# Performance work log

Hardware: AMD Instinct MI355X
Metric: run time of the kernel (lower is better)

Reference implementation:

```python
import jax, jax.numpy as jnp
import numpy as np

NUM_HEADS = 8
ALPHA = 0.01  # leaky_relu slope
MAX_SEQ = 64


def layer_norm(x, g, b, eps=1e-5):
    m = jnp.mean(x, axis=-1, keepdims=True)
    v = jnp.var(x, axis=-1, keepdims=True)
    return (x - m) * jax.lax.rsqrt(v + eps) * g + b


def ff(x, w1, b1, w2, b2):
    # Linear -> exact GELU -> Linear (torch nn.GELU default is erf-based)
    return jax.nn.gelu(x @ w1.T + b1, approximate=False) @ w2.T + b2


def mha(q, k, v, in_w, in_b, out_w, out_b, kpm):
    # torch nn.MultiheadAttention, batch_first=False. q:[Tq,E,d], k/v:[Tk,E,d], kpm:[E,Tk] True=pad
    d = q.shape[-1]
    H = NUM_HEADS
    dh = d // H
    qp = q @ in_w[:d].T + in_b[:d]
    kp = k @ in_w[d:2 * d].T + in_b[d:2 * d]
    vp = v @ in_w[2 * d:].T + in_b[2 * d:]
    Tq, E, _ = qp.shape
    Tk = kp.shape[0]
    qh = qp.reshape(Tq, E, H, dh) * (dh ** -0.5)
    kh = kp.reshape(Tk, E, H, dh)
    vh = vp.reshape(Tk, E, H, dh)
    scores = jnp.einsum('qehd,kehd->ehqk', qh, kh)  # [E,H,Tq,Tk]
    scores = jnp.where(kpm[:, None, None, :], jnp.float32(-1e9), scores)
    att = jax.nn.softmax(scores, axis=-1)
    out = jnp.einsum('ehqk,kehd->qehd', att, vh).reshape(Tq, E, d)
    return out @ out_w.T + out_b


def setup_inputs() -> dict:
    key = jax.random.key(0)
    ks = jax.random.split(key, 40)
    N, d, E, Seq, H = 50000, 64, 150000, 5, NUM_HEADS

    def xn(k, shape, scale):
        return jax.random.normal(k, shape, dtype=jnp.float32) * scale

    inp = {
        'features': xn(ks[0], (N, d), 1.0),
        'pos_emb': xn(ks[1], (MAX_SEQ, d), 0.02),
        'self_in_w': xn(ks[2], (3 * d, d), 0.1),
        'self_in_b': jnp.zeros((3 * d,), jnp.float32),
        'self_out_w': xn(ks[3], (d, d), 0.1),
        'self_out_b': jnp.zeros((d,), jnp.float32),
        'cross_in_w': xn(ks[4], (3 * d, d), 0.1),
        'cross_in_b': jnp.zeros((3 * d,), jnp.float32),
        'cross_out_w': xn(ks[5], (d, d), 0.1),
        'cross_out_b': jnp.zeros((d,), jnp.float32),
        'sa_ln1_g': jnp.ones((d,), jnp.float32), 'sa_ln1_b': jnp.zeros((d,), jnp.float32),
        'sa_ln2_g': jnp.ones((d,), jnp.float32), 'sa_ln2_b': jnp.zeros((d,), jnp.float32),
        'ca_ln1_g': jnp.ones((d,), jnp.float32), 'ca_ln1_b': jnp.zeros((d,), jnp.float32),
        'ca_ln2_g': jnp.ones((d,), jnp.float32), 'ca_ln2_b': jnp.zeros((d,), jnp.float32),
        'sa_ff_w1': xn(ks[6], (4 * d, d), 0.08), 'sa_ff_b1': jnp.zeros((4 * d,), jnp.float32),
        'sa_ff_w2': xn(ks[7], (d, 4 * d), 0.08), 'sa_ff_b2': jnp.zeros((d,), jnp.float32),
        'ca_ff_w1': xn(ks[8], (4 * d, d), 0.08), 'ca_ff_b1': jnp.zeros((4 * d,), jnp.float32),
        'ca_ff_w2': xn(ks[9], (d, 4 * d), 0.08), 'ca_ff_b2': jnp.zeros((d,), jnp.float32),
        'inst_w': xn(ks[10], (NUM_HEADS * d, d), 0.08),
        'attn_vec': xn(ks[11], (1, NUM_HEADS, d), 0.2),
        'edge_metapath_indices': jax.random.randint(ks[12], (E, Seq), 0, N, dtype=jnp.int64)
            if jax.config.jax_enable_x64 else jax.random.randint(ks[12], (E, Seq), 0, N).astype(jnp.int32),
        'dst': jax.random.randint(ks[13], (E,), 0, N).astype(jnp.int32),
    }
    inp['edge_metapath_indices'] = inp['edge_metapath_indices'].astype(jnp.int32)
    return inp


def reference(features, pos_emb, self_in_w, self_in_b, self_out_w, self_out_b,
              cross_in_w, cross_in_b, cross_out_w, cross_out_b,
              sa_ln1_g, sa_ln1_b, sa_ln2_g, sa_ln2_b,
              ca_ln1_g, ca_ln1_b, ca_ln2_g, ca_ln2_b,
              sa_ff_w1, sa_ff_b1, sa_ff_w2, sa_ff_b2,
              ca_ff_w1, ca_ff_b1, ca_ff_w2, ca_ff_b2,
              inst_w, attn_vec, edge_metapath_indices, dst):
    N, d = features.shape
    pad_id = N  # module pads one zero row; indices == pad_id are padding
    feats = jnp.concatenate([features, jnp.zeros((1, d), features.dtype)], axis=0)
    idx = edge_metapath_indices  # [E, Seq]
    E, Seq = idx.shape
    kpm = idx == pad_id  # [E, Seq] key padding mask

    edata = feats[idx]  # [E, Seq, d] gather (embedding)
    tokens = jnp.transpose(edata, (1, 0, 2))  # [Seq, E, d]
    pos_vec = pos_emb[:Seq][:, None, :]  # [Seq, 1, d]
    pos_vec = jnp.where(kpm.T[:, :, None], jnp.float32(0.0), pos_vec)
    tokens = tokens + pos_vec  # pos_drop is identity in eval

    # pre-LN self-attention block over the metapath sequence
    sa_in = layer_norm(tokens, sa_ln1_g, sa_ln1_b)
    tokens = tokens + mha(sa_in, sa_in, sa_in, self_in_w, self_in_b, self_out_w, self_out_b, kpm)
    sa_out = jnp.transpose(tokens, (1, 0, 2))  # [E, Seq, d]

    valid = (~kpm).astype(features.dtype)  # [E, Seq]
    denom = jnp.clip(valid.sum(axis=1, keepdims=True), 1.0, None)
    inst_emb = (sa_out * valid[:, :, None]).sum(axis=1) / denom  # masked mean pool
    inst_emb = inst_emb + ff(layer_norm(inst_emb, sa_ln2_g, sa_ln2_b), sa_ff_w1, sa_ff_b1, sa_ff_w2, sa_ff_b2)

    # cross-attention: last (target) node attends over the sequence
    lengths = (~kpm).sum(axis=1)
    last_pos = jnp.clip(lengths - 1, 0, None)
    last_ids = jnp.take_along_axis(idx, last_pos[:, None], axis=1)[:, 0]
    target_feat = feats[last_ids]
    q = layer_norm(target_feat, ca_ln1_g, ca_ln1_b)[None]  # [1, E, d]
    cross_out = mha(q, tokens, tokens, cross_in_w, cross_in_b, cross_out_w, cross_out_b, kpm)
    inst_emb = inst_emb + cross_out[0]
    inst_emb = inst_emb + ff(layer_norm(inst_emb, ca_ln2_g, ca_ln2_b), ca_ff_w1, ca_ff_b1, ca_ff_w2, ca_ff_b2)

    # heads projection, leaky-relu attention score, edge softmax, scatter-sum
    eft = (inst_emb @ inst_w.T).reshape(E, NUM_HEADS, d)  # [E, H, d]
    a = jnp.sum(eft * attn_vec, axis=-1)  # [E, H]
    a = jnp.where(a > 0, a, ALPHA * a)  # leaky_relu
    seg_max = jax.ops.segment_max(a, dst, num_segments=N)  # per-dst-node max
    a_exp = jnp.exp(a - seg_max[dst])
    seg_sum = jax.ops.segment_sum(a_exp, dst, num_segments=N)
    att = a_exp / seg_sum[dst]  # edge_softmax; attn_drop=0 -> identity
    ret = jax.ops.segment_sum(eft * att[:, :, None], dst, num_segments=N)  # [N, H, d]
    return ret
```

## Files before the change

### kernel.cpp

```cpp
#include <hip/hip_runtime.h>
#include <math.h>

#define D 64
#define LOG2E 1.44269504088896340736f
#define QSCALE (0.35355339059327373f * LOG2E)

typedef float f32x4 __attribute__((ext_vector_type(4)));
typedef float vf4 __attribute__((ext_vector_type(4)));
typedef short bf16x8 __attribute__((ext_vector_type(8)));
typedef unsigned short ushort_t;
typedef unsigned int uint2v __attribute__((ext_vector_type(2)));

#define MF(a, b, c) __builtin_amdgcn_mfma_f32_16x16x32_bf16(a, b, c, 0, 0, 0)

__device__ __forceinline__ float bcast(float x, int i) {
  return __int_as_float(__builtin_amdgcn_readlane(__float_as_int(x), i));
}

__device__ __forceinline__ float xs16(float x) {
#if __has_builtin(__builtin_amdgcn_permlane16_swap)
  uint2v a = __builtin_amdgcn_permlane16_swap(__float_as_uint(x), __float_as_uint(x), false, false);
  return __uint_as_float(a[0]) + __uint_as_float(a[1]);
#else
  return x + __shfl_xor(x, 16);
#endif
}
__device__ __forceinline__ float xs32(float x) {
#if __has_builtin(__builtin_amdgcn_permlane32_swap)
  uint2v a = __builtin_amdgcn_permlane32_swap(__float_as_uint(x), __float_as_uint(x), false, false);
  return __uint_as_float(a[0]) + __uint_as_float(a[1]);
#else
  return x + __shfl_xor(x, 32);
#endif
}
__device__ __forceinline__ float qsum(float x) {
  return xs32(xs16(x));
}

__device__ __forceinline__ ushort_t f2b(float f) {
  unsigned int u = __float_as_uint(f);
  unsigned int r = (u + 0x7FFFu + ((u >> 16) & 1u)) >> 16;
  return (ushort_t)r;
}
__device__ __forceinline__ unsigned int pkrtne(float lo, float hi) {
  unsigned int a = __float_as_uint(lo);
  unsigned int b = __float_as_uint(hi);
  a = a + 0x7FFFu + ((a >> 16) & 1u);
  b = b + 0x7FFFu + ((b >> 16) & 1u);
  return __builtin_amdgcn_perm(b, a, 0x07060302u);
}
__device__ __forceinline__ f32x4 ld4(const float* __restrict__ p) { return *(const f32x4*)p; }
__device__ __forceinline__ bf16x8 mkpair(const f32x4& ce, const f32x4& co) {
  union { bf16x8 v; unsigned int w[4]; } u;
  u.w[0] = pkrtne(ce[0], ce[1]);
  u.w[1] = pkrtne(ce[2], ce[3]);
  u.w[2] = pkrtne(co[0], co[1]);
  u.w[3] = pkrtne(co[2], co[3]);
  return u.v;
}
__device__ __forceinline__ f32x4 unpk(bf16x8 p, int half) {
  union { bf16x8 v; unsigned int w[4]; } u;
  u.v = p;
  unsigned int w0 = u.w[half * 2], w1 = u.w[half * 2 + 1];
  f32x4 r;
  r[0] = __uint_as_float(w0 << 16);
  r[1] = __uint_as_float(w0 & 0xFFFF0000u);
  r[2] = __uint_as_float(w1 << 16);
  r[3] = __uint_as_float(w1 & 0xFFFF0000u);
  return r;
}

__device__ __forceinline__ void lnT(const f32x4 (&x)[4], f32x4 (&y)[4],
                                    const float* __restrict__ g, const float* __restrict__ b,
                                    int quad) {
  float s1 = 0.f, s2 = 0.f;
#pragma unroll
  for (int ct = 0; ct < 4; ct++)
#pragma unroll
    for (int r = 0; r < 4; r++) { s1 += x[ct][r]; s2 += x[ct][r] * x[ct][r]; }
  s1 = qsum(s1);
  s2 = qsum(s2);
  float mean = s1 * 0.015625f;
  float var = s2 * 0.015625f - mean * mean;
  float rs = rsqrtf(var + 1e-5f);
#pragma unroll
  for (int ct = 0; ct < 4; ct++) {
    f32x4 gv = ld4(g + 16 * ct + 4 * quad);
    f32x4 bv = ld4(b + 16 * ct + 4 * quad);
#pragma unroll
    for (int r = 0; r < 4; r++) y[ct][r] = (x[ct][r] - mean) * rs * gv[r] + bv[r];
  }
}

__global__ void prep_kernel(const float* __restrict__ si, const float* __restrict__ so,
                            const float* __restrict__ w1s, const float* __restrict__ w2s,
                            const float* __restrict__ ci, const float* __restrict__ co,
                            const float* __restrict__ w1c, const float* __restrict__ w2c,
                            const float* __restrict__ iw, const float* __restrict__ av,
                            float* __restrict__ ws, unsigned int* __restrict__ zp, int zn) {
  int t = blockIdx.x * blockDim.x + threadIdx.x;
  ushort_t* bw = (ushort_t*)(ws + 33280);
  if (t < 98304) {
    const float* src;
    int base, cs;
    int l = t;
    if      (l < 12288) { src = si;  base = 0;     cs = 6; }
    else if (l < 16384) { src = so;  base = 12288; cs = 6; l -= 12288; }
    else if (l < 32768) { src = w1s; base = 16384; cs = 6; l -= 16384; }
    else if (l < 49152) { src = w2s; base = 32768; cs = 8; l -= 32768; }
    else if (l < 61440) { src = ci;  base = 49152; cs = 6; l -= 49152; }
    else if (l < 65536) { src = co;  base = 61440; cs = 6; l -= 61440; }
    else if (l < 81920) { src = w1c; base = 65536; cs = 6; l -= 65536; }
    else                { src = w2c; base = 81920; cs = 8; l -= 81920; }
    int c = l >> cs, k = l & ((1 << cs) - 1);
    int T = (1 << cs) >> 5;
    int ct = c >> 4, m = c & 15, tt = k >> 5, rem = k & 31;
    int quad = (rem >> 2) & 3;
    int j = (((rem >> 4) & 1) << 2) | (rem & 3);
    bw[base + (size_t)((ct * T + tt) * 64 + quad * 16 + m) * 8 + j] = f2b(src[l]);
  } else if (t < 131072) {
    int l = t - 98304;
    int c = l >> 6, k = l & 63;
    ws[(k >> 2) * 2048 + c * 4 + (k & 3)] = iw[l];
  } else if (t < 131584) {
    int l = t - 131072;
    int h = l >> 6, k = l & 63;
    float acc = 0.f;
    for (int c = 0; c < 64; c++) acc += av[h * 64 + c] * iw[(h * 64 + c) * 64 + k];
    ws[32768 + h * 64 + k] = acc;
  } else if (t - 131584 < zn) {
    zp[t - 131584] = 0u;
  }
}

#define SC1(KARR, QF, CT, KS, P)                                                        \
  { f32x4 kv_ = unpk(KARR[KS][(CT) >> 1], (CT) & 1);                                    \
    float sp_ = QF[CT][0] * kv_[0] + QF[CT][1] * kv_[1] + QF[CT][2] * kv_[2] +          \
                QF[CT][3] * kv_[3];                                                     \
    sp_ = xs16(sp_);                                                                    \
    P = ((vb >> (KS)) & 1) ? sp_ : -1e30f; }

#define PV1(VARR, CT, KS, P, ACC)                                                       \
  { f32x4 vv_ = unpk(VARR[KS][(CT) >> 1], (CT) & 1);                                    \
    _Pragma("unroll") for (int r = 0; r < 4; r++) ACC[r] = fmaf(P, vv_[r], ACC[r]); }

#define ATT_CT(KARR, VARR, QF, CT, OD)                                                  \
  {                                                                                     \
    float p0, p1, p2, p3, p4;                                                           \
    SC1(KARR, QF, CT, 0, p0); SC1(KARR, QF, CT, 1, p1); SC1(KARR, QF, CT, 2, p2);       \
    SC1(KARR, QF, CT, 3, p3); SC1(KARR, QF, CT, 4, p4);                                 \
    float mx_ = fmaxf(fmaxf(fmaxf(p0, p1), fmaxf(p2, p3)), p4);                         \
    p0 = exp2f(p0 - mx_); p1 = exp2f(p1 - mx_); p2 = exp2f(p2 - mx_);                   \
    p3 = exp2f(p3 - mx_); p4 = exp2f(p4 - mx_);                                         \
    float ri_ = 1.0f / (p0 + p1 + p2 + p3 + p4);                                        \
    p0 *= ri_; p1 *= ri_; p2 *= ri_; p3 *= ri_; p4 *= ri_;                              \
    OD = (f32x4){0.f, 0.f, 0.f, 0.f};                                                   \
    PV1(VARR, CT, 0, p0, OD); PV1(VARR, CT, 1, p1, OD); PV1(VARR, CT, 2, p2, OD);       \
    PV1(VARR, CT, 3, p3, OD); PV1(VARR, CT, 4, p4, OD);                                 \
  }

#define KV_STAGE(S)                                                                     \
  {                                                                                     \
    f32x4 t[4], y[4];                                                                   \
    const bool vd = (vb >> (S)) & 1;                                                    \
    const float* fp = features + (size_t)min(ids[S], N - 1) * 64;                       \
    _Pragma("unroll")                                                                   \
    for (int ct = 0; ct < 4; ct++) {                                                    \
      f32x4 f = ld4(fp + 16 * ct + 4 * quad);                                           \
      f32x4 pv = ld4(pos_emb + (S) * 64 + 16 * ct + 4 * quad);                          \
      _Pragma("unroll")                                                                 \
      for (int r = 0; r < 4; r++) t[ct][r] = vd ? (f[r] + pv[r]) : 0.f;                 \
    }                                                                                   \
    lnT(t, y, sa_ln1_g, sa_ln1_b, quad);                                                \
    bf16x8 xl0 = mkpair(y[0], y[1]), xl1 = mkpair(y[2], y[3]);                          \
    f32x4 kt[4], vt[4];                                                                 \
    _Pragma("unroll")                                                                   \
    for (int ct = 0; ct < 4; ct++) {                                                    \
      f32x4 c = {0.f, 0.f, 0.f, 0.f};                                                   \
      c = MF(WSI[((4 + ct) * 2 + 0) * 64 + lane], xl0, c);                              \
      c = MF(WSI[((4 + ct) * 2 + 1) * 64 + lane], xl1, c);                              \
      f32x4 bb = ld4(self_in_b + 64 + 16 * ct + 4 * quad);                              \
      _Pragma("unroll")                                                                 \
      for (int r = 0; r < 4; r++) kt[ct][r] = c[r] + bb[r];                             \
      f32x4 c2 = {0.f, 0.f, 0.f, 0.f};                                                  \
      c2 = MF(WSI[((8 + ct) * 2 + 0) * 64 + lane], xl0, c2);                            \
      c2 = MF(WSI[((8 + ct) * 2 + 1) * 64 + lane], xl1, c2);                            \
      f32x4 bb2 = ld4(self_in_b + 128 + 16 * ct + 4 * quad);                            \
      _Pragma("unroll")                                                                 \
      for (int r = 0; r < 4; r++) vt[ct][r] = c2[r] + bb2[r];                           \
    }                                                                                   \
    Kp[S][0] = mkpair(kt[0], kt[1]); Kp[S][1] = mkpair(kt[2], kt[3]);                   \
    Vp[S][0] = mkpair(vt[0], vt[1]); Vp[S][1] = mkpair(vt[2], vt[3]);                   \
  }

#define Q_STAGE(S)                                                                      \
  {                                                                                     \
    const bool vd = (vb >> (S)) & 1;                                                    \
    const float* fp = features + (size_t)min(ids[S], N - 1) * 64;                       \
    f32x4 t[4], y[4];                                                                   \
    _Pragma("unroll")                                                                   \
    for (int ct = 0; ct < 4; ct++) {                                                    \
      f32x4 f = ld4(fp + 16 * ct + 4 * quad);                                           \
      f32x4 pv = ld4(pos_emb + (S) * 64 + 16 * ct + 4 * quad);                          \
      _Pragma("unroll")                                                                 \
      for (int r = 0; r < 4; r++) t[ct][r] = vd ? (f[r] + pv[r]) : 0.f;                 \
    }                                                                                   \
    lnT(t, y, sa_ln1_g, sa_ln1_b, quad);                                                \
    bf16x8 xl0 = mkpair(y[0], y[1]), xl1 = mkpair(y[2], y[3]);                          \
    f32x4 qf[4];                                                                        \
    _Pragma("unroll")                                                                   \
    for (int ct = 0; ct < 4; ct++) {                                                    \
      f32x4 c = {0.f, 0.f, 0.f, 0.f};                                                   \
      c = MF(WSI[(ct * 2 + 0) * 64 + lane], xl0, c);                                    \
      c = MF(WSI[(ct * 2 + 1) * 64 + lane], xl1, c);                                    \
      f32x4 bb = ld4(self_in_b + 16 * ct + 4 * quad);                                   \
      _Pragma("unroll")                                                                 \
      for (int r = 0; r < 4; r++) qf[ct][r] = (c[r] + bb[r]) * QSCALE;                  \
    }                                                                                   \
    f32x4 oa0, oa1, oa2, oa3;                                                           \
    ATT_CT(Kp, Vp, qf, 0, oa0); ATT_CT(Kp, Vp, qf, 1, oa1);                             \
    ATT_CT(Kp, Vp, qf, 2, oa2); ATT_CT(Kp, Vp, qf, 3, oa3);                             \
    bf16x8 op0 = mkpair(oa0, oa1), op1 = mkpair(oa2, oa3);                              \
    f32x4 tpc[4];                                                                       \
    _Pragma("unroll")                                                                   \
    for (int ct = 0; ct < 4; ct++) {                                                    \
      f32x4 c = {0.f, 0.f, 0.f, 0.f};                                                   \
      c = MF(WSO[(ct * 2 + 0) * 64 + lane], op0, c);                                    \
      c = MF(WSO[(ct * 2 + 1) * 64 + lane], op1, c);                                    \
      f32x4 bb = ld4(self_out_b + 16 * ct + 4 * quad);                                  \
      _Pragma("unroll")                                                                 \
      for (int r = 0; r < 4; r++) {                                                     \
        float tp_ = c[r] + bb[r] + t[ct][r];                                            \
        tpc[ct][r] = tp_;                                                               \
        pool[ct][r] += vd ? tp_ : 0.f;                                                  \
      }                                                                                 \
    }                                                                                   \
    TP[S][0] = mkpair(tpc[0], tpc[1]); TP[S][1] = mkpair(tpc[2], tpc[3]);               \
  }

#define CKV_STAGE(S)                                                                    \
  {                                                                                     \
    f32x4 kt[4], vt[4];                                                                 \
    _Pragma("unroll")                                                                   \
    for (int ct = 0; ct < 4; ct++) {                                                    \
      f32x4 c = {0.f, 0.f, 0.f, 0.f};                                                   \
      c = MF(WCI[((4 + ct) * 2 + 0) * 64 + lane], TP[S][0], c);                         \
      c = MF(WCI[((4 + ct) * 2 + 1) * 64 + lane], TP[S][1], c);                         \
      f32x4 bb = ld4(cross_in_b + 64 + 16 * ct + 4 * quad);                             \
      _Pragma("unroll")                                                                 \
      for (int r = 0; r < 4; r++) kt[ct][r] = c[r] + bb[r];                             \
      f32x4 c2 = {0.f, 0.f, 0.f, 0.f};                                                  \
      c2 = MF(WCI[((8 + ct) * 2 + 0) * 64 + lane], TP[S][0], c2);                       \
      c2 = MF(WCI[((8 + ct) * 2 + 1) * 64 + lane], TP[S][1], c2);                       \
      f32x4 bb2 = ld4(cross_in_b + 128 + 16 * ct + 4 * quad);                           \
      _Pragma("unroll")                                                                 \
      for (int r = 0; r < 4; r++) vt[ct][r] = c2[r] + bb2[r];                           \
    }                                                                                   \
    Kc[S][0] = mkpair(kt[0], kt[1]); Kc[S][1] = mkpair(kt[2], kt[3]);                   \
    Vc[S][0] = mkpair(vt[0], vt[1]); Vc[S][1] = mkpair(vt[2], vt[3]);                   \
  }

#define FF_H2(CT, HD)                                                                   \
  { f32x4 c = {0.f, 0.f, 0.f, 0.f};                                                     \
    c = MF(W1[((CT) * 2 + 0) * 64 + lane], x0, c);                                      \
    c = MF(W1[((CT) * 2 + 1) * 64 + lane], x1, c);                                      \
    f32x4 bb = ld4(b1 + 16 * (CT) + 4 * quad);                                          \
    _Pragma("unroll")                                                                   \
    for (int r = 0; r < 4; r++) {                                                       \
      float v = c[r] + bb[r];                                                           \
      HD[r] = 0.5f * v * (1.0f + erff(v * 0.70710678118654752440f));                    \
    } }

#define FF_O(CT)                                                                        \
  { f32x4 c = {0.f, 0.f, 0.f, 0.f};                                                     \
    c = MF(W2[((CT) * 8 + 0) * 64 + lane], Hp0, c);                                     \
    c = MF(W2[((CT) * 8 + 1) * 64 + lane], Hp1, c);                                     \
    c = MF(W2[((CT) * 8 + 2) * 64 + lane], Hp2, c);                                     \
    c = MF(W2[((CT) * 8 + 3) * 64 + lane], Hp3, c);                                     \
    c = MF(W2[((CT) * 8 + 4) * 64 + lane], Hp4, c);                                     \
    c = MF(W2[((CT) * 8 + 5) * 64 + lane], Hp5, c);                                     \
    c = MF(W2[((CT) * 8 + 6) * 64 + lane], Hp6, c);                                     \
    c = MF(W2[((CT) * 8 + 7) * 64 + lane], Hp7, c);                                     \
    f32x4 bb = ld4(b2 + 16 * (CT) + 4 * quad);                                          \
    _Pragma("unroll")                                                                   \
    for (int r = 0; r < 4; r++) inst[CT][r] += c[r] + bb[r]; }

__device__ __forceinline__ void ffnT(f32x4 (&inst)[4],
                                     const float* __restrict__ g, const float* __restrict__ b,
                                     const bf16x8* __restrict__ W1, const bf16x8* __restrict__ W2,
                                     const float* __restrict__ b1, const float* __restrict__ b2,
                                     int lane, int quad) {
  f32x4 y[4];
  lnT(inst, y, g, b, quad);
  bf16x8 x0 = mkpair(y[0], y[1]), x1 = mkpair(y[2], y[3]);
  f32x4 ha, hb;
  FF_H2(0, ha);  FF_H2(1, hb);  bf16x8 Hp0 = mkpair(ha, hb);
  FF_H2(2, ha);  FF_H2(3, hb);  bf16x8 Hp1 = mkpair(ha, hb);
  FF_H2(4, ha);  FF_H2(5, hb);  bf16x8 Hp2 = mkpair(ha, hb);
  FF_H2(6, ha);  FF_H2(7, hb);  bf16x8 Hp3 = mkpair(ha, hb);
  FF_H2(8, ha);  FF_H2(9, hb);  bf16x8 Hp4 = mkpair(ha, hb);
  FF_H2(10, ha); FF_H2(11, hb); bf16x8 Hp5 = mkpair(ha, hb);
  FF_H2(12, ha); FF_H2(13, hb); bf16x8 Hp6 = mkpair(ha, hb);
  FF_H2(14, ha); FF_H2(15, hb); bf16x8 Hp7 = mkpair(ha, hb);
  FF_O(0); FF_O(1); FF_O(2); FF_O(3);
}

#define ASC(H)                                                                          \
  { float sp = 0.f;                                                                     \
    _Pragma("unroll")                                                                   \
    for (int ct = 0; ct < 4; ct++) {                                                    \
      f32x4 uu = ld4(uvec + (H) * 64 + 16 * ct + 4 * quad);                             \
      _Pragma("unroll")                                                                 \
      for (int r = 0; r < 4; r++) sp = fmaf(inst[ct][r], uu[r], sp);                    \
    }                                                                                   \
    sp = qsum(sp);                                                                      \
    a##H = sp > 0.f ? sp : 0.01f * sp; }

__global__ __launch_bounds__(64, 1)
void edge_kernel(const float* __restrict__ features, const float* __restrict__ pos_emb,
                 const float* __restrict__ self_in_b, const float* __restrict__ self_out_b,
                 const float* __restrict__ cross_in_b, const float* __restrict__ cross_out_b,
                 const float* __restrict__ sa_ln1_g, const float* __restrict__ sa_ln1_b,
                 const float* __restrict__ sa_ln2_g, const float* __restrict__ sa_ln2_b,
                 const float* __restrict__ ca_ln1_g, const float* __restrict__ ca_ln1_b,
                 const float* __restrict__ ca_ln2_g, const float* __restrict__ ca_ln2_b,
                 const float* __restrict__ sa_ff_b1, const float* __restrict__ sa_ff_b2,
                 const float* __restrict__ ca_ff_b1, const float* __restrict__ ca_ff_b2,
                 const int* __restrict__ midx, const int* __restrict__ dstv,
                 const float* __restrict__ ws,
                 float* __restrict__ inst_out, float* __restrict__ a_out, int E, int N) {
  const int lane = threadIdx.x;
  const int quad = lane >> 4, lo = lane & 15;
  const int e0 = blockIdx.x * 16;
  __shared__ float xp[16 * 68];

  const ushort_t* bw = (const ushort_t*)(ws + 33280);
  const bf16x8* WSI = (const bf16x8*)(bw);
  const bf16x8* WSO = (const bf16x8*)(bw + 12288);
  const bf16x8* W1S = (const bf16x8*)(bw + 16384);
  const bf16x8* W2S = (const bf16x8*)(bw + 32768);
  const bf16x8* WCI = (const bf16x8*)(bw + 49152);
  const bf16x8* WCO = (const bf16x8*)(bw + 61440);
  const bf16x8* W1C = (const bf16x8*)(bw + 65536);
  const bf16x8* W2C = (const bf16x8*)(bw + 81920);
  const float* uvec = ws + 32768;

  const bool ge = (e0 + lo) < E;
  const int eIdx = min(e0 + lo, E - 1);
  int ids[5];
  ids[0] = midx[eIdx * 5 + 0];
  ids[1] = midx[eIdx * 5 + 1];
  ids[2] = midx[eIdx * 5 + 2];
  ids[3] = midx[eIdx * 5 + 3];
  ids[4] = midx[eIdx * 5 + 4];
  int vb = 0;
  if (ids[0] != N && ge) vb |= 1;
  if (ids[1] != N && ge) vb |= 2;
  if (ids[2] != N && ge) vb |= 4;
  if (ids[3] != N && ge) vb |= 8;
  if (ids[4] != N && ge) vb |= 16;
  const int nv = __popc(vb);
  const int lp = max(nv - 1, 0);
  int lid = ids[0];
  lid = (lp == 1) ? ids[1] : lid;
  lid = (lp == 2) ? ids[2] : lid;
  lid = (lp == 3) ? ids[3] : lid;
  lid = (lp == 4) ? ids[4] : lid;

  bf16x8 Kp[5][2], Vp[5][2];
  KV_STAGE(0); KV_STAGE(1); KV_STAGE(2); KV_STAGE(3); KV_STAGE(4);

  f32x4 pool[4];
#pragma unroll
  for (int ct = 0; ct < 4; ct++) pool[ct] = (f32x4){0.f, 0.f, 0.f, 0.f};
  bf16x8 TP[5][2];
  Q_STAGE(0); Q_STAGE(1); Q_STAGE(2); Q_STAGE(3); Q_STAGE(4);

  f32x4 inst[4];
  {
    float rn = 1.0f / (float)max(nv, 1);
#pragma unroll
    for (int ct = 0; ct < 4; ct++)
#pragma unroll
      for (int r = 0; r < 4; r++) inst[ct][r] = pool[ct][r] * rn;
  }

  ffnT(inst, sa_ln2_g, sa_ln2_b, W1S, W2S, sa_ff_b1, sa_ff_b2, lane, quad);

  {
    f32x4 tf[4], xq[4];
    const bool vdl = lid != N;
    const float* fp = features + (size_t)min(lid, N - 1) * 64;
#pragma unroll
    for (int ct = 0; ct < 4; ct++) {
      f32x4 f = ld4(fp + 16 * ct + 4 * quad);
#pragma unroll
      for (int r = 0; r < 4; r++) tf[ct][r] = vdl ? f[r] : 0.f;
    }
    lnT(tf, xq, ca_ln1_g, ca_ln1_b, quad);
    bf16x8 xq0 = mkpair(xq[0], xq[1]), xq1 = mkpair(xq[2], xq[3]);
    f32x4 qcf[4];
#pragma unroll
    for (int ct = 0; ct < 4; ct++) {
      f32x4 c = {0.f, 0.f, 0.f, 0.f};
      c = MF(WCI[(ct * 2 + 0) * 64 + lane], xq0, c);
      c = MF(WCI[(ct * 2 + 1) * 64 + lane], xq1, c);
      f32x4 bb = ld4(cross_in_b + 16 * ct + 4 * quad);
#pragma unroll
      for (int r = 0; r < 4; r++) qcf[ct][r] = (c[r] + bb[r]) * QSCALE;
    }
    bf16x8 Kc[5][2], Vc[5][2];
    CKV_STAGE(0); CKV_STAGE(1); CKV_STAGE(2); CKV_STAGE(3); CKV_STAGE(4);
    f32x4 cc0, cc1, cc2, cc3;
    ATT_CT(Kc, Vc, qcf, 0, cc0); ATT_CT(Kc, Vc, qcf, 1, cc1);
    ATT_CT(Kc, Vc, qcf, 2, cc2); ATT_CT(Kc, Vc, qcf, 3, cc3);
    bf16x8 cp0 = mkpair(cc0, cc1), cp1 = mkpair(cc2, cc3);
#pragma unroll
    for (int ct = 0; ct < 4; ct++) {
      f32x4 c = {0.f, 0.f, 0.f, 0.f};
      c = MF(WCO[(ct * 2 + 0) * 64 + lane], cp0, c);
      c = MF(WCO[(ct * 2 + 1) * 64 + lane], cp1, c);
      f32x4 bb = ld4(cross_out_b + 16 * ct + 4 * quad);
#pragma unroll
      for (int r = 0; r < 4; r++) inst[ct][r] += c[r] + bb[r];
    }
  }

  ffnT(inst, ca_ln2_g, ca_ln2_b, W1C, W2C, ca_ff_b1, ca_ff_b2, lane, quad);

  float a0, a1, a2, a3, a4, a5, a6, a7;
  ASC(0); ASC(1); ASC(2); ASC(3); ASC(4); ASC(5); ASC(6); ASC(7);
  if (ge && quad < 2) {
    f32x4 st = (quad == 0) ? (f32x4){a0, a1, a2, a3} : (f32x4){a4, a5, a6, a7};
    *(f32x4*)(a_out + (size_t)(e0 + lo) * 8 + 4 * quad) = st;
  }

#pragma unroll
  for (int ct = 0; ct < 4; ct++)
    *(f32x4*)(&xp[lo * 68 + 16 * ct + 4 * quad]) = inst[ct];
  __syncthreads();
  {
    int er = lane >> 2, cb = (lane & 3) * 16;
    if (e0 + er < E) {
#pragma unroll
      for (int u = 0; u < 4; u++) {
        f32x4 v = *(const f32x4*)(&xp[er * 68 + cb + 4 * u]);
        *(f32x4*)(inst_out + (size_t)(e0 + er) * 64 + cb + 4 * u) = v;
      }
    }
  }
}

__global__ void csr_count_kernel(const int* __restrict__ dstv, unsigned int* __restrict__ cnt,
                                 int E) {
  int e = blockIdx.x * blockDim.x + threadIdx.x;
  if (e < E) atomicAdd(&cnt[dstv[e]], 1u);
}

__global__ void scan1_kernel(unsigned int* __restrict__ off, unsigned int* __restrict__ bsum,
                             int N) {
  __shared__ unsigned int sd[256];
  int t = threadIdx.x, n = blockIdx.x * 256 + t;
  unsigned int v = (n < N) ? off[n] : 0u;
  sd[t] = v;
  __syncthreads();
  for (int o = 1; o < 256; o <<= 1) {
    unsigned int x = (t >= o) ? sd[t - o] : 0u;
    __syncthreads();
    sd[t] += x;
    __syncthreads();
  }
  if (n < N) off[n] = sd[t] - v;
  if (t == 255) bsum[blockIdx.x] = sd[255];
}

__global__ void scan2_kernel(unsigned int* __restrict__ bsum, int nb) {
  __shared__ unsigned int sd[1024];
  int t = threadIdx.x;
  unsigned int v = (t < nb) ? bsum[t] : 0u;
  sd[t] = v;
  __syncthreads();
  for (int o = 1; o < 1024; o <<= 1) {
    unsigned int x = (t >= o) ? sd[t - o] : 0u;
    __syncthreads();
    sd[t] += x;
    __syncthreads();
  }
  if (t < nb) bsum[t] = sd[t] - v;
}

__global__ void scan3_kernel(unsigned int* __restrict__ off, unsigned int* __restrict__ cur,
                             const unsigned int* __restrict__ bsum, int N, int E) {
  int n = blockIdx.x * 256 + threadIdx.x;
  if (n < N) {
    unsigned int o = off[n] + bsum[blockIdx.x];
    off[n] = o;
    cur[n] = o;
  }
  if (n == 0) off[N] = (unsigned int)E;
}

__global__ void csr_fill_kernel(const int* __restrict__ dstv, unsigned int* __restrict__ cur,
                                unsigned int* __restrict__ elist, int E) {
  int e = blockIdx.x * blockDim.x + threadIdx.x;
  if (e < E) {
    unsigned int p = atomicAdd(&cur[dstv[e]], 1u);
    elist[p] = (unsigned int)e;
  }
}

__global__ __launch_bounds__(256)
void att_kernel(const unsigned int* __restrict__ off, const unsigned int* __restrict__ elist,
                float* __restrict__ a, float* __restrict__ sinv, int N) {
  int n = blockIdx.x * blockDim.x + threadIdx.x;
  if (n >= N) return;
  const unsigned int s0 = off[n], s1 = off[n + 1];
  f32x4 m0 = {-3.0e38f, -3.0e38f, -3.0e38f, -3.0e38f}, m1 = m0;
  for (unsigned int i = s0; i < s1; i++) {
    const float* ap = a + (size_t)elist[i] * 8;
    f32x4 x0 = ld4(ap), x1 = ld4(ap + 4);
#pragma unroll
    for (int r = 0; r < 4; r++) { m0[r] = fmaxf(m0[r], x0[r]); m1[r] = fmaxf(m1[r], x1[r]); }
  }
  f32x4 t0 = {0.f, 0.f, 0.f, 0.f}, t1 = t0;
  for (unsigned int i = s0; i < s1; i++) {
    float* ap = a + (size_t)elist[i] * 8;
    f32x4 x0 = ld4(ap), x1 = ld4(ap + 4);
    f32x4 w0, w1;
#pragma unroll
    for (int r = 0; r < 4; r++) {
      w0[r] = __expf(x0[r] - m0[r]);
      w1[r] = __expf(x1[r] - m1[r]);
      t0[r] += w0[r];
      t1[r] += w1[r];
    }
    *(f32x4*)ap = w0;
    *(f32x4*)(ap + 4) = w1;
  }
  f32x4 r0, r1;
#pragma unroll
  for (int r = 0; r < 4; r++) {
    r0[r] = (t0[r] > 0.f) ? 1.0f / t0[r] : 0.f;
    r1[r] = (t1[r] > 0.f) ? 1.0f / t1[r] : 0.f;
  }
  *(f32x4*)(sinv + (size_t)n * 8) = r0;
  *(f32x4*)(sinv + (size_t)n * 8 + 4) = r1;
}

__global__ __launch_bounds__(256)
void gather_kernel(const float* __restrict__ T_iw, const unsigned int* __restrict__ off,
                   const unsigned int* __restrict__ elist, const float* __restrict__ a,
                   const float* __restrict__ sinv, const float* __restrict__ inst_emb,
                   float* __restrict__ out, int N) {
  const int lane = threadIdx.x & 63;
  const int widx = threadIdx.x >> 6;
  const int h = blockIdx.y;
  const vf4* P = (const vf4*)T_iw;
  vf4 wr[16];
#pragma unroll
  for (int k = 0; k < 16; k++) wr[k] = P[k * 512 + h * 64 + lane];
  const int stride = gridDim.x * 4;
  for (int n = blockIdx.x * 4 + widx; n < N; n += stride) {
    const unsigned int s0 = off[n], s1 = off[n + 1];
    float z = 0.f;
    for (unsigned int i = s0; i < s1; i++) {
      unsigned int e = elist[i];
      z = fmaf(a[(size_t)e * 8 + h], inst_emb[(size_t)e * 64 + lane], z);
    }
    z *= sinv[(size_t)n * 8 + h];
    float o = 0.f;
#pragma unroll
    for (int k = 0; k < 16; k++) {
#pragma unroll
      for (int u = 0; u < 4; u++) o = fmaf(bcast(z, k * 4 + u), wr[k][u], o);
    }
    out[(size_t)n * 512 + h * 64 + lane] = o;
  }
}

extern "C" void kernel_launch(void* const* d_in, const int* in_sizes, int n_in,
                              void* d_out, int out_size, void* d_ws, size_t ws_size,
                              hipStream_t stream) {
  const float* features   = (const float*)d_in[0];
  const float* pos_emb    = (const float*)d_in[1];
  const float* self_in_w  = (const float*)d_in[2];
  const float* self_in_b  = (const float*)d_in[3];
  const float* self_out_w = (const float*)d_in[4];
  const float* self_out_b = (const float*)d_in[5];
  const float* cross_in_w = (const float*)d_in[6];
  const float* cross_in_b = (const float*)d_in[7];
  const float* cross_out_w= (const float*)d_in[8];
  const float* cross_out_b= (const float*)d_in[9];
  const float* sa_ln1_g = (const float*)d_in[10];
  const float* sa_ln1_b = (const float*)d_in[11];
  const float* sa_ln2_g = (const float*)d_in[12];
  const float* sa_ln2_b = (const float*)d_in[13];
  const float* ca_ln1_g = (const float*)d_in[14];
  const float* ca_ln1_b = (const float*)d_in[15];
  const float* ca_ln2_g = (const float*)d_in[16];
  const float* ca_ln2_b = (const float*)d_in[17];
  const float* sa_ff_w1 = (const float*)d_in[18];
  const float* sa_ff_b1 = (const float*)d_in[19];
  const float* sa_ff_w2 = (const float*)d_in[20];
  const float* sa_ff_b2 = (const float*)d_in[21];
  const float* ca_ff_w1 = (const float*)d_in[22];
  const float* ca_ff_b1 = (const float*)d_in[23];
  const float* ca_ff_w2 = (const float*)d_in[24];
  const float* ca_ff_b2 = (const float*)d_in[25];
  const float* inst_w   = (const float*)d_in[26];
  const float* attn_vec = (const float*)d_in[27];
  const int* midx = (const int*)d_in[28];
  const int* dstv = (const int*)d_in[29];

  const int N = in_sizes[0] / 64;
  const int E = in_sizes[29];

  float* wsf = (float*)d_ws;
  float* inst_emb = wsf + 131072;
  float* a_arr = inst_emb + (size_t)E * 64;
  unsigned int* off = (unsigned int*)(a_arr + (size_t)E * 8);
  unsigned int* cur = off + (size_t)(N + 1);
  unsigned int* bsum = cur + (size_t)N;
  unsigned int* elist = bsum + 1024;
  float* sinv = (float*)(elist + (size_t)E);

  const int nb1 = (N + 255) / 256;

  int zn = N + 1;
  prep_kernel<<<(131584 + zn + 255) / 256, 256, 0, stream>>>(
      self_in_w, self_out_w, sa_ff_w1, sa_ff_w2, cross_in_w, cross_out_w, ca_ff_w1, ca_ff_w2,
      inst_w, attn_vec, wsf, off, zn);

  csr_count_kernel<<<(E + 255) / 256, 256, 0, stream>>>(dstv, off, E);
  scan1_kernel<<<nb1, 256, 0, stream>>>(off, bsum, N);
  scan2_kernel<<<1, 1024, 0, stream>>>(bsum, nb1);
  scan3_kernel<<<nb1, 256, 0, stream>>>(off, cur, bsum, N, E);
  csr_fill_kernel<<<(E + 255) / 256, 256, 0, stream>>>(dstv, cur, elist, E);

  int nblk = (E + 15) / 16;
  edge_kernel<<<nblk, 64, 0, stream>>>(
      features, pos_emb, self_in_b, self_out_b, cross_in_b, cross_out_b, sa_ln1_g, sa_ln1_b,
      sa_ln2_g, sa_ln2_b, ca_ln1_g, ca_ln1_b, ca_ln2_g, ca_ln2_b, sa_ff_b1, sa_ff_b2, ca_ff_b1,
      ca_ff_b2, midx, dstv, wsf, inst_emb, a_arr, E, N);

  att_kernel<<<(N + 255) / 256, 256, 0, stream>>>(off, elist, a_arr, sinv, N);

  dim3 ggrid(256, 8);
  gather_kernel<<<ggrid, 256, 0, stream>>>(wsf, off, elist, a_arr, sinv, inst_emb,
                                           (float*)d_out, N);
}
```

Before: 921.7 us.

## Process two 16-edge tiles per wavefront in edge kernel to reuse weight fragments

The fused edge kernel now handles 32 edges per 64-thread block, computing two independent 16-edge tiles (A and B) side by side. Each weight fragment loaded from the workspace is reused for two MFMA chains, and the interleaved independent work gives the scheduler more latency hiding. The grid is halved to match. The cost is roughly doubled register pressure, which may lower occupancy or cause spills, plus an extra shared-memory round trip and barrier for the second tile's output.

```diff
diff --git a/kernel.cpp b/kernel.cpp
--- a/kernel.cpp
+++ b/kernel.cpp
@@ -90,6 +90,25 @@
 #pragma unroll
     for (int r = 0; r < 4; r++) y[ct][r] = (x[ct][r] - mean) * rs * gv[r] + bv[r];
   }
+}
+
+__device__ __forceinline__ void gatherLN(const float* __restrict__ features,
+                                         const float* __restrict__ pos_emb, int id, bool vd,
+                                         int S, const float* __restrict__ g,
+                                         const float* __restrict__ b, int quad,
+                                         f32x4 (&t)[4], bf16x8& x0, bf16x8& x1, int N) {
+  f32x4 y[4];
+  const float* fp = features + (size_t)min(id, N - 1) * 64;
+#pragma unroll
+  for (int ct = 0; ct < 4; ct++) {
+    f32x4 f = ld4(fp + 16 * ct + 4 * quad);
+    f32x4 pv = ld4(pos_emb + S * 64 + 16 * ct + 4 * quad);
+#pragma unroll
+    for (int r = 0; r < 4; r++) t[ct][r] = vd ? (f[r] + pv[r]) : 0.f;
+  }
+  lnT(t, y, g, b, quad);
+  x0 = mkpair(y[0], y[1]);
+  x1 = mkpair(y[2], y[3]);
 }
 
 __global__ void prep_kernel(const float* __restrict__ si, const float* __restrict__ so,
@@ -133,22 +152,23 @@
   }
 }
 
-#define SC1(KARR, QF, CT, KS, P)                                                        \
+#define SC1(KARR, QF, CT, KS, P, VB)                                                    \
   { f32x4 kv_ = unpk(KARR[KS][(CT) >> 1], (CT) & 1);                                    \
     float sp_ = QF[CT][0] * kv_[0] + QF[CT][1] * kv_[1] + QF[CT][2] * kv_[2] +          \
                 QF[CT][3] * kv_[3];                                                     \
     sp_ = xs16(sp_);                                                                    \
-    P = ((vb >> (KS)) & 1) ? sp_ : -1e30f; }
+    P = (((VB) >> (KS)) & 1) ? sp_ : -1e30f; }
 
 #define PV1(VARR, CT, KS, P, ACC)                                                       \
   { f32x4 vv_ = unpk(VARR[KS][(CT) >> 1], (CT) & 1);                                    \
     _Pragma("unroll") for (int r = 0; r < 4; r++) ACC[r] = fmaf(P, vv_[r], ACC[r]); }
 
-#define ATT_CT(KARR, VARR, QF, CT, OD)                                                  \
+#define ATT_CT(KARR, VARR, QF, CT, OD, VB)                                              \
   {                                                                                     \
     float p0, p1, p2, p3, p4;                                                           \
-    SC1(KARR, QF, CT, 0, p0); SC1(KARR, QF, CT, 1, p1); SC1(KARR, QF, CT, 2, p2);       \
-    SC1(KARR, QF, CT, 3, p3); SC1(KARR, QF, CT, 4, p4);                                 \
+    SC1(KARR, QF, CT, 0, p0, VB); SC1(KARR, QF, CT, 1, p1, VB);                         \
+    SC1(KARR, QF, CT, 2, p2, VB); SC1(KARR, QF, CT, 3, p3, VB);                         \
+    SC1(KARR, QF, CT, 4, p4, VB);                                                       \
     float mx_ = fmaxf(fmaxf(fmaxf(p0, p1), fmaxf(p2, p3)), p4);                         \
     p0 = exp2f(p0 - mx_); p1 = exp2f(p1 - mx_); p2 = exp2f(p2 - mx_);                   \
     p3 = exp2f(p3 - mx_); p4 = exp2f(p4 - mx_);                                         \
@@ -159,162 +179,196 @@
     PV1(VARR, CT, 3, p3, OD); PV1(VARR, CT, 4, p4, OD);                                 \
   }
 
-#define KV_STAGE(S)                                                                     \
+#define KV2(S)                                                                          \
   {                                                                                     \
-    f32x4 t[4], y[4];                                                                   \
-    const bool vd = (vb >> (S)) & 1;                                                    \
-    const float* fp = features + (size_t)min(ids[S], N - 1) * 64;                       \
+    f32x4 tA[4], tB[4];                                                                 \
+    bf16x8 xA0, xA1, xB0, xB1;                                                          \
+    gatherLN(features, pos_emb, idsA[S], (vbA >> (S)) & 1, (S), sa_ln1_g, sa_ln1_b,     \
+             quad, tA, xA0, xA1, N);                                                    \
+    gatherLN(features, pos_emb, idsB[S], (vbB >> (S)) & 1, (S), sa_ln1_g, sa_ln1_b,     \
+             quad, tB, xB0, xB1, N);                                                    \
+    f32x4 ktA[4], vtA[4], ktB[4], vtB[4];                                               \
     _Pragma("unroll")                                                                   \
     for (int ct = 0; ct < 4; ct++) {                                                    \
-      f32x4 f = ld4(fp + 16 * ct + 4 * quad);                                           \
-      f32x4 pv = ld4(pos_emb + (S) * 64 + 16 * ct + 4 * quad);                          \
-      _Pragma("unroll")                                                                 \
-      for (int r = 0; r < 4; r++) t[ct][r] = vd ? (f[r] + pv[r]) : 0.f;                 \
+      bf16x8 wk0 = WSI[((4 + ct) * 2 + 0) * 64 + lane];                                 \
+      bf16x8 wk1 = WSI[((4 + ct) * 2 + 1) * 64 + lane];                                 \
+      bf16x8 wv0 = WSI[((8 + ct) * 2 + 0) * 64 + lane];                                 \
+      bf16x8 wv1 = WSI[((8 + ct) * 2 + 1) * 64 + lane];                                 \
+      f32x4 bbk = ld4(self_in_b + 64 + 16 * ct + 4 * quad);                             \
+      f32x4 bbv = ld4(self_in_b + 128 + 16 * ct + 4 * quad);                            \
+      f32x4 c = {0.f, 0.f, 0.f, 0.f};                                                   \
+      c = MF(wk0, xA0, c); c = MF(wk1, xA1, c);                                         \
+      _Pragma("unroll") for (int r = 0; r < 4; r++) ktA[ct][r] = c[r] + bbk[r];         \
+      c = (f32x4){0.f, 0.f, 0.f, 0.f};                                                  \
+      c = MF(wk0, xB0, c); c = MF(wk1, xB1, c);                                         \
+      _Pragma("unroll") for (int r = 0; r < 4; r++) ktB[ct][r] = c[r] + bbk[r];         \
+      c = (f32x4){0.f, 0.f, 0.f, 0.f};                                                  \
+      c = MF(wv0, xA0, c); c = MF(wv1, xA1, c);                                         \
+      _Pragma("unroll") for (int r = 0; r < 4; r++) vtA[ct][r] = c[r] + bbv[r];         \
+      c = (f32x4){0.f, 0.f, 0.f, 0.f};                                                  \
+      c = MF(wv0, xB0, c); c = MF(wv1, xB1, c);                                         \
+      _Pragma("unroll") for (int r = 0; r < 4; r++) vtB[ct][r] = c[r] + bbv[r];         \
     }                                                                                   \
-    lnT(t, y, sa_ln1_g, sa_ln1_b, quad);                                                \
-    bf16x8 xl0 = mkpair(y[0], y[1]), xl1 = mkpair(y[2], y[3]);                          \
-    f32x4 kt[4], vt[4];                                                                 \
+    KpA[S][0] = mkpair(ktA[0], ktA[1]); KpA[S][1] = mkpair(ktA[2], ktA[3]);             \
+    VpA[S][0] = mkpair(vtA[0], vtA[1]); VpA[S][1] = mkpair(vtA[2], vtA[3]);             \
+    KpB[S][0] = mkpair(ktB[0], ktB[1]); KpB[S][1] = mkpair(ktB[2], ktB[3]);             \
+    VpB[S][0] = mkpair(vtB[0], vtB[1]); VpB[S][1] = mkpair(vtB[2], vtB[3]);             \
+  }
+
+#define Q2(S)                                                                           \
+  {                                                                                     \
+    f32x4 tA[4], tB[4];                                                                 \
+    bf16x8 xA0, xA1, xB0, xB1;                                                          \
+    gatherLN(features, pos_emb, idsA[S], (vbA >> (S)) & 1, (S), sa_ln1_g, sa_ln1_b,     \
+             quad, tA, xA0, xA1, N);                                                    \
+    gatherLN(features, pos_emb, idsB[S], (vbB >> (S)) & 1, (S), sa_ln1_g, sa_ln1_b,     \
+             quad, tB, xB0, xB1, N);                                                    \
+    f32x4 qfA[4], qfB[4];                                                               \
     _Pragma("unroll")                                                                   \
     for (int ct = 0; ct < 4; ct++) {                                                    \
+      bf16x8 w0 = WSI[(ct * 2 + 0) * 64 + lane];                                        \
+      bf16x8 w1 = WSI[(ct * 2 + 1) * 64 + lane];                                        \
+      f32x4 bb = ld4(self_in_b + 16 * ct + 4 * quad);                                   \
       f32x4 c = {0.f, 0.f, 0.f, 0.f};                                                   \
-      c = MF(WSI[((4 + ct) * 2 + 0) * 64 + lane], xl0, c);                              \
-      c = MF(WSI[((4 + ct) * 2 + 1) * 64 + lane], xl1, c);                              \
-      f32x4 bb = ld4(self_in_b + 64 + 16 * ct + 4 * quad);                              \
-      _Pragma("unroll")                                                                 \
-      for (int r = 0; r < 4; r++) kt[ct][r] = c[r] + bb[r];                             \
-      f32x4 c2 = {0.f, 0.f, 0.f, 0.f};                                                  \
-      c2 = MF(WSI[((8 + ct) * 2 + 0) * 64 + lane], xl0, c2);                            \
-      c2 = MF(WSI[((8 + ct) * 2 + 1) * 64 + lane], xl1, c2);                            \
-      f32x4 bb2 = ld4(self_in_b + 128 + 16 * ct + 4 * quad);                            \
-      _Pragma("unroll")                                                                 \
-      for (int r = 0; r < 4; r++) vt[ct][r] = c2[r] + bb2[r];                           \
+      c = MF(w0, xA0, c); c = MF(w1, xA1, c);                                           \
+      _Pragma("unroll") for (int r = 0; r < 4; r++) qfA[ct][r] = (c[r] + bb[r]) * QSCALE; \
+      c = (f32x4){0.f, 0.f, 0.f, 0.f};                                                  \
+      c = MF(w0, xB0, c); c = MF(w1, xB1, c);                                           \
+      _Pragma("unroll") for (int r = 0; r < 4; r++) qfB[ct][r] = (c[r] + bb[r]) * QSCALE; \
     }                                                                                   \
-    Kp[S][0] = mkpair(kt[0], kt[1]); Kp[S][1] = mkpair(kt[2], kt[3]);                   \
-    Vp[S][0] = mkpair(vt[0], vt[1]); Vp[S][1] = mkpair(vt[2], vt[3]);                   \
-  }
-
-#define Q_STAGE(S)                                                                      \
-  {                                                                                     \
-    const bool vd = (vb >> (S)) & 1;                                                    \
-    const float* fp = features + (size_t)min(ids[S], N - 1) * 64;                       \
-    f32x4 t[4], y[4];                                                                   \
+    f32x4 oA0, oA1, oA2, oA3, oB0, oB1, oB2, oB3;                                       \
+    ATT_CT(KpA, VpA, qfA, 0, oA0, vbA); ATT_CT(KpA, VpA, qfA, 1, oA1, vbA);             \
+    ATT_CT(KpA, VpA, qfA, 2, oA2, vbA); ATT_CT(KpA, VpA, qfA, 3, oA3, vbA);             \
+    ATT_CT(KpB, VpB, qfB, 0, oB0, vbB); ATT_CT(KpB, VpB, qfB, 1, oB1, vbB);             \
+    ATT_CT(KpB, VpB, qfB, 2, oB2, vbB); ATT_CT(KpB, VpB, qfB, 3, oB3, vbB);             \
+    bf16x8 opA0 = mkpair(oA0, oA1), opA1 = mkpair(oA2, oA3);                            \
+    bf16x8 opB0 = mkpair(oB0, oB1), opB1 = mkpair(oB2, oB3);                            \
+    const bool vdA = (vbA >> (S)) & 1, vdB = (vbB >> (S)) & 1;                          \
+    f32x4 tpA[4], tpB[4];                                                               \
     _Pragma("unroll")                                                                   \
     for (int ct = 0; ct < 4; ct++) {                                                    \
-      f32x4 f = ld4(fp + 16 * ct + 4 * quad);                                           \
-      f32x4 pv = ld4(pos_emb + (S) * 64 + 16 * ct + 4 * quad);                          \
-      _Pragma("unroll")                                                                 \
-      for (int r = 0; r < 4; r++) t[ct][r] = vd ? (f[r] + pv[r]) : 0.f;                 \
+      bf16x8 w0 = WSO[(ct * 2 + 0) * 64 + lane];                                        \
+      bf16x8 w1 = WSO[(ct * 2 + 1) * 64 + lane];                                        \
+      f32x4 bb = ld4(self_out_b + 16 * ct + 4 * quad);                                  \
+      f32x4 c = {0.f, 0.f, 0.f, 0.f};                                                   \
+      c = MF(w0, opA0, c); c = MF(w1, opA1, c);                                         \
+      _Pragma("unroll") for (int r = 0; r < 4; r++) {                                   \
+        float tp_ = c[r] + bb[r] + tA[ct][r];                                           \
+        tpA[ct][r] = tp_;                                                               \
+        poolA[ct][r] += vdA ? tp_ : 0.f;                                                \
+      }                                                                                 \
+      c = (f32x4){0.f, 0.f, 0.f, 0.f};                                                  \
+      c = MF(w0, opB0, c); c = MF(w1, opB1, c);                                         \
+      _Pragma("unroll") for (int r = 0; r < 4; r++) {                                   \
+        float tp_ = c[r] + bb[r] + tB[ct][r];                                           \
+        tpB[ct][r] = tp_;                                                               \
+        poolB[ct][r] += vdB ? tp_ : 0.f;                                                \
+      }                                                                                 \
     }                                                                                   \
-    lnT(t, y, sa_ln1_g, sa_ln1_b, quad);                                                \
-    bf16x8 xl0 = mkpair(y[0], y[1]), xl1 = mkpair(y[2], y[3]);                          \
-    f32x4 qf[4];                                                                        \
+    TPA[S][0] = mkpair(tpA[0], tpA[1]); TPA[S][1] = mkpair(tpA[2], tpA[3]);             \
+    TPB[S][0] = mkpair(tpB[0], tpB[1]); TPB[S][1] = mkpair(tpB[2], tpB[3]);             \
+  }
+
+#define CKV2(S)                                                                         \
+  {                                                                                     \
+    f32x4 ktA[4], vtA[4], ktB[4], vtB[4];                                               \
     _Pragma("unroll")                                                                   \
     for (int ct = 0; ct < 4; ct++) {                                                    \
+      bf16x8 wk0 = WCI[((4 + ct) * 2 + 0) * 64 + lane];                                 \
+      bf16x8 wk1 = WCI[((4 + ct) * 2 + 1) * 64 + lane];                                 \
+      bf16x8 wv0 = WCI[((8 + ct) * 2 + 0) * 64 + lane];                                 \
+      bf16x8 wv1 = WCI[((8 + ct) * 2 + 1) * 64 + lane];                                 \
+      f32x4 bbk = ld4(cross_in_b + 64 + 16 * ct + 4 * quad);                            \
+      f32x4 bbv = ld4(cross_in_b + 128 + 16 * ct + 4 * quad);                           \
       f32x4 c = {0.f, 0.f, 0.f, 0.f};                                                   \
-      c = MF(WSI[(ct * 2 + 0) * 64 + lane], xl0, c);                                    \
-      c = MF(WSI[(ct * 2 + 1) * 64 + lane], xl1, c);                                    \
-      f32x4 bb = ld4(self_in_b + 16 * ct + 4 * quad);                                   \
-      _Pragma("unroll")                                                                 \
-      for (int r = 0; r < 4; r++) qf[ct][r] = (c[r] + bb[r]) * QSCALE;                  \
+      c = MF(wk0, TPA[S][0], c); c = MF(wk1, TPA[S][1], c);                             \
+      _Pragma("unroll") for (int r = 0; r < 4; r++) ktA[ct][r] = c[r] + bbk[r];         \
+      c = (f32x4){0.f, 0.f, 0.f, 0.f};                                                  \
+      c = MF(wk0, TPB[S][0], c); c = MF(wk1, TPB[S][1], c);                             \
+      _Pragma("unroll") for (int r = 0; r < 4; r++) ktB[ct][r] = c[r] + bbk[r];         \
+      c = (f32x4){0.f, 0.f, 0.f, 0.f};                                                  \
+      c = MF(wv0, TPA[S][0], c); c = MF(wv1, TPA[S][1], c);                             \
+      _Pragma("unroll") for (int r = 0; r < 4; r++) vtA[ct][r] = c[r] + bbv[r];         \
+      c = (f32x4){0.f, 0.f, 0.f, 0.f};                                                  \
+      c = MF(wv0, TPB[S][0], c); c = MF(wv1, TPB[S][1], c);                             \
+      _Pragma("unroll") for (int r = 0; r < 4; r++) vtB[ct][r] = c[r] + bbv[r];         \
     }                                                                                   \
-    f32x4 oa0, oa1, oa2, oa3;                                                           \
-    ATT_CT(Kp, Vp, qf, 0, oa0); ATT_CT(Kp, Vp, qf, 1, oa1);                             \
-    ATT_CT(Kp, Vp, qf, 2, oa2); ATT_CT(Kp, Vp, qf, 3, oa3);                             \
-    bf16x8 op0 = mkpair(oa0, oa1), op1 = mkpair(oa2, oa3);                              \
-    f32x4 tpc[4];                                                                       \
-    _Pragma("unroll")                                                                   \
-    for (int ct = 0; ct < 4; ct++) {                                                    \
-      f32x4 c = {0.f, 0.f, 0.f, 0.f};                                                   \
-      c = MF(WSO[(ct * 2 + 0) * 64 + lane], op0, c);                                    \
-      c = MF(WSO[(ct * 2 + 1) * 64 + lane], op1, c);                                    \
-      f32x4 bb = ld4(self_out_b + 16 * ct + 4 * quad);                                  \
-      _Pragma("unroll")                                                                 \
-      for (int r = 0; r < 4; r++) {                                                     \
-        float tp_ = c[r] + bb[r] + t[ct][r];                                            \
-        tpc[ct][r] = tp_;                                                               \
-        pool[ct][r] += vd ? tp_ : 0.f;                                                  \
-      }                                                                                 \
-    }                                                                                   \
-    TP[S][0] = mkpair(tpc[0], tpc[1]); TP[S][1] = mkpair(tpc[2], tpc[3]);               \
-  }
-
-#define CKV_STAGE(S)                                                                    \
-  {                                                                                     \
-    f32x4 kt[4], vt[4];                                                                 \
-    _Pragma("unroll")                                                                   \
-    for (int ct = 0; ct < 4; ct++) {                                                    \
-      f32x4 c = {0.f, 0.f, 0.f, 0.f};                                                   \
-      c = MF(WCI[((4 + ct) * 2 + 0) * 64 + lane], TP[S][0], c);                         \
-      c = MF(WCI[((4 + ct) * 2 + 1) * 64 + lane], TP[S][1], c);                         \
-      f32x4 bb = ld4(cross_in_b + 64 + 16 * ct + 4 * quad);                             \
-      _Pragma("unroll")                                                                 \
-      for (int r = 0; r < 4; r++) kt[ct][r] = c[r] + bb[r];                             \
-      f32x4 c2 = {0.f, 0.f, 0.f, 0.f};                                                  \
-      c2 = MF(WCI[((8 + ct) * 2 + 0) * 64 + lane], TP[S][0], c2);                       \
-      c2 = MF(WCI[((8 + ct) * 2 + 1) * 64 + lane], TP[S][1], c2);                       \
-      f32x4 bb2 = ld4(cross_in_b + 128 + 16 * ct + 4 * quad);                           \
-      _Pragma("unroll")                                                                 \
-      for (int r = 0; r < 4; r++) vt[ct][r] = c2[r] + bb2[r];                           \
-    }                                                                                   \
-    Kc[S][0] = mkpair(kt[0], kt[1]); Kc[S][1] = mkpair(kt[2], kt[3]);                   \
-    Vc[S][0] = mkpair(vt[0], vt[1]); Vc[S][1] = mkpair(vt[2], vt[3]);                   \
-  }
-
-#define FF_H2(CT, HD)                                                                   \
-  { f32x4 c = {0.f, 0.f, 0.f, 0.f};                                                     \
-    c = MF(W1[((CT) * 2 + 0) * 64 + lane], x0, c);                                      \
-    c = MF(W1[((CT) * 2 + 1) * 64 + lane], x1, c);                                      \
-    f32x4 bb = ld4(b1 + 16 * (CT) + 4 * quad);                                          \
-    _Pragma("unroll")                                                                   \
-    for (int r = 0; r < 4; r++) {                                                       \
-      float v = c[r] + bb[r];                                                           \
-      HD[r] = 0.5f * v * (1.0f + erff(v * 0.70710678118654752440f));                    \
-    } }
-
-#define FF_O(CT)                                                                        \
-  { f32x4 c = {0.f, 0.f, 0.f, 0.f};                                                     \
-    c = MF(W2[((CT) * 8 + 0) * 64 + lane], Hp0, c);                                     \
-    c = MF(W2[((CT) * 8 + 1) * 64 + lane], Hp1, c);                                     \
-    c = MF(W2[((CT) * 8 + 2) * 64 + lane], Hp2, c);                                     \
-    c = MF(W2[((CT) * 8 + 3) * 64 + lane], Hp3, c);                                     \
-    c = MF(W2[((CT) * 8 + 4) * 64 + lane], Hp4, c);                                     \
-    c = MF(W2[((CT) * 8 + 5) * 64 + lane], Hp5, c);                                     \
-    c = MF(W2[((CT) * 8 + 6) * 64 + lane], Hp6, c);                                     \
-    c = MF(W2[((CT) * 8 + 7) * 64 + lane], Hp7, c);                                     \
-    f32x4 bb = ld4(b2 + 16 * (CT) + 4 * quad);                                          \
-    _Pragma("unroll")                                                                   \
-    for (int r = 0; r < 4; r++) inst[CT][r] += c[r] + bb[r]; }
-
-__device__ __forceinline__ void ffnT(f32x4 (&inst)[4],
-                                     const float* __restrict__ g, const float* __restrict__ b,
-                                     const bf16x8* __restrict__ W1, const bf16x8* __restrict__ W2,
-                                     const float* __restrict__ b1, const float* __restrict__ b2,
-                                     int lane, int quad) {
-  f32x4 y[4];
-  lnT(inst, y, g, b, quad);
-  bf16x8 x0 = mkpair(y[0], y[1]), x1 = mkpair(y[2], y[3]);
-  f32x4 ha, hb;
-  FF_H2(0, ha);  FF_H2(1, hb);  bf16x8 Hp0 = mkpair(ha, hb);
-  FF_H2(2, ha);  FF_H2(3, hb);  bf16x8 Hp1 = mkpair(ha, hb);
-  FF_H2(4, ha);  FF_H2(5, hb);  bf16x8 Hp2 = mkpair(ha, hb);
-  FF_H2(6, ha);  FF_H2(7, hb);  bf16x8 Hp3 = mkpair(ha, hb);
-  FF_H2(8, ha);  FF_H2(9, hb);  bf16x8 Hp4 = mkpair(ha, hb);
-  FF_H2(10, ha); FF_H2(11, hb); bf16x8 Hp5 = mkpair(ha, hb);
-  FF_H2(12, ha); FF_H2(13, hb); bf16x8 Hp6 = mkpair(ha, hb);
-  FF_H2(14, ha); FF_H2(15, hb); bf16x8 Hp7 = mkpair(ha, hb);
-  FF_O(0); FF_O(1); FF_O(2); FF_O(3);
-}
-
-#define ASC(H)                                                                          \
-  { float sp = 0.f;                                                                     \
+    KcA[S][0] = mkpair(ktA[0], ktA[1]); KcA[S][1] = mkpair(ktA[2], ktA[3]);             \
+    VcA[S][0] = mkpair(vtA[0], vtA[1]); VcA[S][1] = mkpair(vtA[2], vtA[3]);             \
+    KcB[S][0] = mkpair(ktB[0], ktB[1]); KcB[S][1] = mkpair(ktB[2], ktB[3]);             \
+    VcB[S][0] = mkpair(vtB[0], vtB[1]); VcB[S][1] = mkpair(vtB[2], vtB[3]);             \
+  }
+
+__device__ __forceinline__ void ffnT2(f32x4 (&iA)[4], f32x4 (&iB)[4],
+                                      const float* __restrict__ g, const float* __restrict__ b,
+                                      const bf16x8* __restrict__ W1, const bf16x8* __restrict__ W2,
+                                      const float* __restrict__ b1, const float* __restrict__ b2,
+                                      int lane, int quad) {
+  f32x4 yA[4], yB[4];
+  lnT(iA, yA, g, b, quad);
+  lnT(iB, yB, g, b, quad);
+  bf16x8 xA0 = mkpair(yA[0], yA[1]), xA1 = mkpair(yA[2], yA[3]);
+  bf16x8 xB0 = mkpair(yB[0], yB[1]), xB1 = mkpair(yB[2], yB[3]);
+  bf16x8 HA[8], HB[8];
+#pragma unroll
+  for (int ht = 0; ht < 8; ht++) {
+    f32x4 hA[2], hB[2];
+#pragma unroll
+    for (int u = 0; u < 2; u++) {
+      int ct = 2 * ht + u;
+      bf16x8 w0 = W1[(ct * 2 + 0) * 64 + lane];
+      bf16x8 w1 = W1[(ct * 2 + 1) * 64 + lane];
+      f32x4 bb = ld4(b1 + 16 * ct + 4 * quad);
+      f32x4 c = {0.f, 0.f, 0.f, 0.f};
+      c = MF(w0, xA0, c); c = MF(w1, xA1, c);
+#pragma unroll
+      for (int r = 0; r < 4; r++) {
+        float v = c[r] + bb[r];
+        hA[u][r] = 0.5f * v * (1.0f + erff(v * 0.70710678118654752440f));
+      }
+      c = (f32x4){0.f, 0.f, 0.f, 0.f};
+      c = MF(w0, xB0, c); c = MF(w1, xB1, c);
+#pragma unroll
+      for (int r = 0; r < 4; r++) {
+        float v = c[r] + bb[r];
+        hB[u][r] = 0.5f * v * (1.0f + erff(v * 0.70710678118654752440f));
+      }
+    }
+    HA[ht] = mkpair(hA[0], hA[1]);
+    HB[ht] = mkpair(hB[0], hB[1]);
+  }
+#pragma unroll
+  for (int ct = 0; ct < 4; ct++) {
+    f32x4 cA = {0.f, 0.f, 0.f, 0.f}, cB = {0.f, 0.f, 0.f, 0.f};
+#pragma unroll
+    for (int t = 0; t < 8; t++) {
+      bf16x8 w = W2[(ct * 8 + t) * 64 + lane];
+      cA = MF(w, HA[t], cA);
+      cB = MF(w, HB[t], cB);
+    }
+    f32x4 bb = ld4(b2 + 16 * ct + 4 * quad);
+#pragma unroll
+    for (int r = 0; r < 4; r++) {
+      iA[ct][r] += cA[r] + bb[r];
+      iB[ct][r] += cB[r] + bb[r];
+    }
+  }
+}
+
+#define ASC2(H)                                                                         \
+  { float spA = 0.f, spB = 0.f;                                                         \
     _Pragma("unroll")                                                                   \
     for (int ct = 0; ct < 4; ct++) {                                                    \
       f32x4 uu = ld4(uvec + (H) * 64 + 16 * ct + 4 * quad);                             \
       _Pragma("unroll")                                                                 \
-      for (int r = 0; r < 4; r++) sp = fmaf(inst[ct][r], uu[r], sp);                    \
+      for (int r = 0; r < 4; r++) {                                                     \
+        spA = fmaf(instA[ct][r], uu[r], spA);                                           \
+        spB = fmaf(instB[ct][r], uu[r], spB);                                           \
+      }                                                                                 \
     }                                                                                   \
-    sp = qsum(sp);                                                                      \
-    a##H = sp > 0.f ? sp : 0.01f * sp; }
+    spA = qsum(spA); spB = qsum(spB);                                                   \
+    aA##H = spA > 0.f ? spA : 0.01f * spA;                                              \
+    aB##H = spB > 0.f ? spB : 0.01f * spB; }
 
 __global__ __launch_bounds__(64, 1)
 void edge_kernel(const float* __restrict__ features, const float* __restrict__ pos_emb,
@@ -331,7 +385,7 @@
                  float* __restrict__ inst_out, float* __restrict__ a_out, int E, int N) {
   const int lane = threadIdx.x;
   const int quad = lane >> 4, lo = lane & 15;
-  const int e0 = blockIdx.x * 16;
+  const int e0 = blockIdx.x * 32;
   __shared__ float xp[16 * 68];
 
   const ushort_t* bw = (const ushort_t*)(ws + 33280);
@@ -345,99 +399,148 @@
   const bf16x8* W2C = (const bf16x8*)(bw + 81920);
   const float* uvec = ws + 32768;
 
-  const bool ge = (e0 + lo) < E;
-  const int eIdx = min(e0 + lo, E - 1);
-  int ids[5];
-  ids[0] = midx[eIdx * 5 + 0];
-  ids[1] = midx[eIdx * 5 + 1];
-  ids[2] = midx[eIdx * 5 + 2];
-  ids[3] = midx[eIdx * 5 + 3];
-  ids[4] = midx[eIdx * 5 + 4];
-  int vb = 0;
-  if (ids[0] != N && ge) vb |= 1;
-  if (ids[1] != N && ge) vb |= 2;
-  if (ids[2] != N && ge) vb |= 4;
-  if (ids[3] != N && ge) vb |= 8;
-  if (ids[4] != N && ge) vb |= 16;
-  const int nv = __popc(vb);
-  const int lp = max(nv - 1, 0);
-  int lid = ids[0];
-  lid = (lp == 1) ? ids[1] : lid;
-  lid = (lp == 2) ? ids[2] : lid;
-  lid = (lp == 3) ? ids[3] : lid;
-  lid = (lp == 4) ? ids[4] : lid;
-
-  bf16x8 Kp[5][2], Vp[5][2];
-  KV_STAGE(0); KV_STAGE(1); KV_STAGE(2); KV_STAGE(3); KV_STAGE(4);
-
-  f32x4 pool[4];
-#pragma unroll
-  for (int ct = 0; ct < 4; ct++) pool[ct] = (f32x4){0.f, 0.f, 0.f, 0.f};
-  bf16x8 TP[5][2];
-  Q_STAGE(0); Q_STAGE(1); Q_STAGE(2); Q_STAGE(3); Q_STAGE(4);
-
-  f32x4 inst[4];
+  const bool geA = (e0 + lo) < E;
+  const bool geB = (e0 + 16 + lo) < E;
+  const int eIdxA = min(e0 + lo, E - 1);
+  const int eIdxB = min(e0 + 16 + lo, E - 1);
+  int idsA[5], idsB[5];
+  idsA[0] = midx[eIdxA * 5 + 0];
+  idsA[1] = midx[eIdxA * 5 + 1];
+  idsA[2] = midx[eIdxA * 5 + 2];
+  idsA[3] = midx[eIdxA * 5 + 3];
+  idsA[4] = midx[eIdxA * 5 + 4];
+  idsB[0] = midx[eIdxB * 5 + 0];
+  idsB[1] = midx[eIdxB * 5 + 1];
+  idsB[2] = midx[eIdxB * 5 + 2];
+  idsB[3] = midx[eIdxB * 5 + 3];
+  idsB[4] = midx[eIdxB * 5 + 4];
+  int vbA = 0, vbB = 0;
+  if (idsA[0] != N && geA) vbA |= 1;
+  if (idsA[1] != N && geA) vbA |= 2;
+  if (idsA[2] != N && geA) vbA |= 4;
+  if (idsA[3] != N && geA) vbA |= 8;
+  if (idsA[4] != N && geA) vbA |= 16;
+  if (idsB[0] != N && geB) vbB |= 1;
+  if (idsB[1] != N && geB) vbB |= 2;
+  if (idsB[2] != N && geB) vbB |= 4;
+  if (idsB[3] != N && geB) vbB |= 8;
+  if (idsB[4] != N && geB) vbB |= 16;
+  const int nvA = __popc(vbA), nvB = __popc(vbB);
+  const int lpA = max(nvA - 1, 0), lpB = max(nvB - 1, 0);
+  int lidA = idsA[0];
+  lidA = (lpA == 1) ? idsA[1] : lidA;
+  lidA = (lpA == 2) ? idsA[2] : lidA;
+  lidA = (lpA == 3) ? idsA[3] : lidA;
+  lidA = (lpA == 4) ? idsA[4] : lidA;
+  int lidB = idsB[0];
+  lidB = (lpB == 1) ? idsB[1] : lidB;
+  lidB = (lpB == 2) ? idsB[2] : lidB;
+  lidB = (lpB == 3) ? idsB[3] : lidB;
+  lidB = (lpB == 4) ? idsB[4] : lidB;
+
+  bf16x8 KpA[5][2], VpA[5][2], KpB[5][2], VpB[5][2];
+  KV2(0); KV2(1); KV2(2); KV2(3); KV2(4);
+
+  f32x4 poolA[4], poolB[4];
+#pragma unroll
+  for (int ct = 0; ct < 4; ct++) {
+    poolA[ct] = (f32x4){0.f, 0.f, 0.f, 0.f};
+    poolB[ct] = (f32x4){0.f, 0.f, 0.f, 0.f};
+  }
+  bf16x8 TPA[5][2], TPB[5][2];
+  Q2(0); Q2(1); Q2(2); Q2(3); Q2(4);
+
+  f32x4 instA[4], instB[4];
   {
-    float rn = 1.0f / (float)max(nv, 1);
+    float rnA = 1.0f / (float)max(nvA, 1);
+    float rnB = 1.0f / (float)max(nvB, 1);
 #pragma unroll
     for (int ct = 0; ct < 4; ct++)
 #pragma unroll
-      for (int r = 0; r < 4; r++) inst[ct][r] = pool[ct][r] * rn;
-  }
-
-  ffnT(inst, sa_ln2_g, sa_ln2_b, W1S, W2S, sa_ff_b1, sa_ff_b2, lane, quad);
+      for (int r = 0; r < 4; r++) {
+        instA[ct][r] = poolA[ct][r] * rnA;
+        instB[ct][r] = poolB[ct][r] * rnB;
+      }
+  }
+
+  ffnT2(instA, instB, sa_ln2_g, sa_ln2_b, W1S, W2S, sa_ff_b1, sa_ff_b2, lane, quad);
 
   {
-    f32x4 tf[4], xq[4];
-    const bool vdl = lid != N;
-    const float* fp = features + (size_t)min(lid, N - 1) * 64;
+    f32x4 tfA[4], tfB[4], xqA[4], xqB[4];
+    const bool vdlA = lidA != N, vdlB = lidB != N;
+    const float* fpA = features + (size_t)min(lidA, N - 1) * 64;
+    const float* fpB = features + (size_t)min(lidB, N - 1) * 64;
 #pragma unroll
     for (int ct = 0; ct < 4; ct++) {
-      f32x4 f = ld4(fp + 16 * ct + 4 * quad);
-#pragma unroll
-      for (int r = 0; r < 4; r++) tf[ct][r] = vdl ? f[r] : 0.f;
-    }
-    lnT(tf, xq, ca_ln1_g, ca_ln1_b, quad);
-    bf16x8 xq0 = mkpair(xq[0], xq[1]), xq1 = mkpair(xq[2], xq[3]);
-    f32x4 qcf[4];
+      f32x4 fA = ld4(fpA + 16 * ct + 4 * quad);
+      f32x4 fB = ld4(fpB + 16 * ct + 4 * quad);
+#pragma unroll
+      for (int r = 0; r < 4; r++) {
+        tfA[ct][r] = vdlA ? fA[r] : 0.f;
+        tfB[ct][r] = vdlB ? fB[r] : 0.f;
+      }
+    }
+    lnT(tfA, xqA, ca_ln1_g, ca_ln1_b, quad);
+    lnT(tfB, xqB, ca_ln1_g, ca_ln1_b, quad);
+    bf16x8 xqA0 = mkpair(xqA[0], xqA[1]), xqA1 = mkpair(xqA[2], xqA[3]);
+    bf16x8 xqB0 = mkpair(xqB[0], xqB[1]), xqB1 = mkpair(xqB[2], xqB[3]);
+    f32x4 qcA[4], qcB[4];
 #pragma unroll
     for (int ct = 0; ct < 4; ct++) {
+      bf16x8 w0 = WCI[(ct * 2 + 0) * 64 + lane];
+      bf16x8 w1 = WCI[(ct * 2 + 1) * 64 + lane];
+      f32x4 bb = ld4(cross_in_b + 16 * ct + 4 * quad);
       f32x4 c = {0.f, 0.f, 0.f, 0.f};
-      c = MF(WCI[(ct * 2 + 0) * 64 + lane], xq0, c);
-      c = MF(WCI[(ct * 2 + 1) * 64 + lane], xq1, c);
-      f32x4 bb = ld4(cross_in_b + 16 * ct + 4 * quad);
-#pragma unroll
-      for (int r = 0; r < 4; r++) qcf[ct][r] = (c[r] + bb[r]) * QSCALE;
-    }
-    bf16x8 Kc[5][2], Vc[5][2];
-    CKV_STAGE(0); CKV_STAGE(1); CKV_STAGE(2); CKV_STAGE(3); CKV_STAGE(4);
-    f32x4 cc0, cc1, cc2, cc3;
-    ATT_CT(Kc, Vc, qcf, 0, cc0); ATT_CT(Kc, Vc, qcf, 1, cc1);
-    ATT_CT(Kc, Vc, qcf, 2, cc2); ATT_CT(Kc, Vc, qcf, 3, cc3);
-    bf16x8 cp0 = mkpair(cc0, cc1), cp1 = mkpair(cc2, cc3);
+      c = MF(w0, xqA0, c); c = MF(w1, xqA1, c);
+#pragma unroll
+      for (int r = 0; r < 4; r++) qcA[ct][r] = (c[r] + bb[r]) * QSCALE;
+      c = (f32x4){0.f, 0.f, 0.f, 0.f};
+      c = MF(w0, xqB0, c); c = MF(w1, xqB1, c);
+#pragma unroll
+      for (int r = 0; r < 4; r++) qcB[ct][r] = (c[r] + bb[r]) * QSCALE;
+    }
+    bf16x8 KcA[5][2], VcA[5][2], KcB[5][2], VcB[5][2];
+    CKV2(0); CKV2(1); CKV2(2); CKV2(3); CKV2(4);
+    f32x4 ccA0, ccA1, ccA2, ccA3, ccB0, ccB1, ccB2, ccB3;
+    ATT_CT(KcA, VcA, qcA, 0, ccA0, vbA); ATT_CT(KcA, VcA, qcA, 1, ccA1, vbA);
+    ATT_CT(KcA, VcA, qcA, 2, ccA2, vbA); ATT_CT(KcA, VcA, qcA, 3, ccA3, vbA);
+    ATT_CT(KcB, VcB, qcB, 0, ccB0, vbB); ATT_CT(KcB, VcB, qcB, 1, ccB1, vbB);
+    ATT_CT(KcB, VcB, qcB, 2, ccB2, vbB); ATT_CT(KcB, VcB, qcB, 3, ccB3, vbB);
+    bf16x8 cpA0 = mkpair(ccA0, ccA1), cpA1 = mkpair(ccA2, ccA3);
+    bf16x8 cpB0 = mkpair(ccB0, ccB1), cpB1 = mkpair(ccB2, ccB3);
 #pragma unroll
     for (int ct = 0; ct < 4; ct++) {
+      bf16x8 w0 = WCO[(ct * 2 + 0) * 64 + lane];
+      bf16x8 w1 = WCO[(ct * 2 + 1) * 64 + lane];
+      f32x4 bb = ld4(cross_out_b + 16 * ct + 4 * quad);
       f32x4 c = {0.f, 0.f, 0.f, 0.f};
-      c = MF(WCO[(ct * 2 + 0) * 64 + lane], cp0, c);
-      c = MF(WCO[(ct * 2 + 1) * 64 + lane], cp1, c);
-      f32x4 bb = ld4(cross_out_b + 16 * ct + 4 * quad);
-#pragma unroll
-      for (int r = 0; r < 4; r++) inst[ct][r] += c[r] + bb[r];
-    }
-  }
-
-  ffnT(inst, ca_ln2_g, ca_ln2_b, W1C, W2C, ca_ff_b1, ca_ff_b2, lane, quad);
-
-  float a0, a1, a2, a3, a4, a5, a6, a7;
-  ASC(0); ASC(1); ASC(2); ASC(3); ASC(4); ASC(5); ASC(6); ASC(7);
-  if (ge && quad < 2) {
-    f32x4 st = (quad == 0) ? (f32x4){a0, a1, a2, a3} : (f32x4){a4, a5, a6, a7};
+      c = MF(w0, cpA0, c); c = MF(w1, cpA1, c);
+#pragma unroll
+      for (int r = 0; r < 4; r++) instA[ct][r] += c[r] + bb[r];
+      c = (f32x4){0.f, 0.f, 0.f, 0.f};
+      c = MF(w0, cpB0, c); c = MF(w1, cpB1, c);
+#pragma unroll
+      for (int r = 0; r < 4; r++) instB[ct][r] += c[r] + bb[r];
+    }
+  }
+
+  ffnT2(instA, instB, ca_ln2_g, ca_ln2_b, W1C, W2C, ca_ff_b1, ca_ff_b2, lane, quad);
+
+  float aA0, aA1, aA2, aA3, aA4, aA5, aA6, aA7;
+  float aB0, aB1, aB2, aB3, aB4, aB5, aB6, aB7;
+  ASC2(0); ASC2(1); ASC2(2); ASC2(3); ASC2(4); ASC2(5); ASC2(6); ASC2(7);
+  if (geA && quad < 2) {
+    f32x4 st = (quad == 0) ? (f32x4){aA0, aA1, aA2, aA3} : (f32x4){aA4, aA5, aA6, aA7};
     *(f32x4*)(a_out + (size_t)(e0 + lo) * 8 + 4 * quad) = st;
   }
+  if (geB && quad < 2) {
+    f32x4 st = (quad == 0) ? (f32x4){aB0, aB1, aB2, aB3} : (f32x4){aB4, aB5, aB6, aB7};
+    *(f32x4*)(a_out + (size_t)(e0 + 16 + lo) * 8 + 4 * quad) = st;
+  }
 
 #pragma unroll
   for (int ct = 0; ct < 4; ct++)
-    *(f32x4*)(&xp[lo * 68 + 16 * ct + 4 * quad]) = inst[ct];
+    *(f32x4*)(&xp[lo * 68 + 16 * ct + 4 * quad]) = instA[ct];
   __syncthreads();
   {
     int er = lane >> 2, cb = (lane & 3) * 16;
@@ -446,6 +549,21 @@
       for (int u = 0; u < 4; u++) {
         f32x4 v = *(const f32x4*)(&xp[er * 68 + cb + 4 * u]);
         *(f32x4*)(inst_out + (size_t)(e0 + er) * 64 + cb + 4 * u) = v;
+      }
+    }
+  }
+  __syncthreads();
+#pragma unroll
+  for (int ct = 0; ct < 4; ct++)
+    *(f32x4*)(&xp[lo * 68 + 16 * ct + 4 * quad]) = instB[ct];
+  __syncthreads();
+  {
+    int er = lane >> 2, cb = (lane & 3) * 16;
+    if (e0 + 16 + er < E) {
+#pragma unroll
+      for (int u = 0; u < 4; u++) {
+        f32x4 v = *(const f32x4*)(&xp[er * 68 + cb + 4 * u]);
+        *(f32x4*)(inst_out + (size_t)(e0 + 16 + er) * 64 + cb + 4 * u) = v;
       }
     }
   }
@@ -637,7 +755,7 @@
   scan3_kernel<<<nb1, 256, 0, stream>>>(off, cur, bsum, N, E);
   csr_fill_kernel<<<(E + 255) / 256, 256, 0, stream>>>(dstv, cur, elist, E);
 
-  int nblk = (E + 15) / 16;
+  int nblk = (E + 31) / 32;
   edge_kernel<<<nblk, 64, 0, stream>>>(
       features, pos_emb, self_in_b, self_out_b, cross_in_b, cross_out_b, sa_ln1_g, sa_ln1_b,
       sa_ln2_g, sa_ln2_b, ca_ln1_g, ca_ln1_b, ca_ln2_g, ca_ln2_b, sa_ff_b1, sa_ff_b2, ca_ff_b1,
```

Measured after the change: 1.296 ms. 40.6% more time.
